# Kernel tuning notes

Measured on AMD Instinct MI355X. Metric: run time of the kernel, lower is better.

The kernel has to match this reference:

```python
import jax, jax.numpy as jnp
import numpy as np

B, S, N, D, H = 2, 64, 48, 128, 8
DH = D // H
_SCALE = 1.0 / float(np.sqrt(DH))


def _ln(x, g, b):
    m = jnp.mean(x, -1, keepdims=True)
    v = jnp.mean((x - m) ** 2, -1, keepdims=True)
    return (x - m) * jax.lax.rsqrt(v + 1e-5) * g + b


def setup_inputs() -> dict:
    key = jax.random.key(0)
    ks = jax.random.split(key, 40)
    rn = lambda i, shape, s=0.02: jax.random.normal(ks[i], shape, dtype=jnp.float32) * s
    inp = {
        'x': jax.random.normal(ks[0], (B, S, N, D), dtype=jnp.float32),
        'adjacency_matrix': jax.random.uniform(ks[1], (N, N), dtype=jnp.float32),
        'spatial_pos': rn(2, (1, N, D)),
        'temporal_pos': rn(3, (1, S, D)),
        'inter_w': rn(4, (H, DH, DH)),
        'conv_w1': rn(5, (D, D, 1)), 'conv_b1': jnp.zeros((D,), jnp.float32),
        'conv_w3': rn(6, (D, D, 3)), 'conv_b3': jnp.zeros((D,), jnp.float32),
        'conv_w5': rn(7, (D, D, 5)), 'conv_b5': jnp.zeros((D,), jnp.float32),
        'conv_w7': rn(8, (D, D, 7)), 'conv_b7': jnp.zeros((D,), jnp.float32),
        'sp_w0': rn(9, (D, D)), 'sp_b0': jnp.zeros((D,), jnp.float32),
        'sp_w1': rn(10, (D, D)), 'sp_b1': jnp.zeros((D,), jnp.float32),
        'sp_w2': rn(11, (D, D)), 'sp_b2': jnp.zeros((D,), jnp.float32),
        'attn_in_w': rn(12, (3 * D, D)), 'attn_in_b': jnp.zeros((3 * D,), jnp.float32),
        'attn_out_w': rn(13, (D, D)), 'attn_out_b': jnp.zeros((D,), jnp.float32),
        'gsp_w': rn(14, (D, 2 * D)), 'gsp_b': jnp.zeros((D,), jnp.float32),
        'gtm_w': rn(15, (D, 2 * D)), 'gtm_b': jnp.zeros((D,), jnp.float32),
        'gfu_w': rn(16, (D, 2 * D)), 'gfu_b': jnp.zeros((D,), jnp.float32),
        'ln1_g': jnp.ones((D,), jnp.float32), 'ln1_b': jnp.zeros((D,), jnp.float32),
        'ln2_g': jnp.ones((D,), jnp.float32), 'ln2_b': jnp.zeros((D,), jnp.float32),
        'ln3_g': jnp.ones((D,), jnp.float32), 'ln3_b': jnp.zeros((D,), jnp.float32),
    }
    return inp


def _forward(x, adjacency_matrix, spatial_pos, temporal_pos, inter_w,
             conv_w1, conv_b1, conv_w3, conv_b3, conv_w5, conv_b5, conv_w7, conv_b7,
             sp_w0, sp_b0, sp_w1, sp_b1, sp_w2, sp_b2,
             attn_in_w, attn_in_b, attn_out_w, attn_out_b,
             gsp_w, gsp_b, gtm_w, gtm_b, gfu_w, gfu_b,
             ln1_g, ln1_b, ln2_g, ln2_b, ln3_g, ln3_b):
    # positional encodings: spatial [1,N,D] broadcast over seq, temporal [1,S,D] over nodes
    x = x + spatial_pos[:, None] + temporal_pos[:, :, None]

    # ---- multi-scale temporal conv: [B*N, D, S] conv1d with k in {1,3,5,7} ----
    xt = x.transpose(0, 2, 3, 1).reshape(B * N, D, S)
    acc = None
    for w, b, k in ((conv_w1, conv_b1, 1), (conv_w3, conv_b3, 3), (conv_w5, conv_b5, 5), (conv_w7, conv_b7, 7)):
        o = jax.lax.conv_general_dilated(xt, w, (1,), [(k // 2, k // 2)],
                                         dimension_numbers=('NCH', 'OIH', 'NCH'))
        o = jax.nn.relu(o + b[None, :, None])
        acc = o if acc is None else acc + o
    tmp = (acc / 4.0).reshape(B, N, D, S).transpose(0, 3, 1, 2)  # [B,S,N,D]
    temporal = _ln(tmp + x, ln1_g, ln1_b)

    # ---- multi-hop spatial graph conv ----
    deg = adjacency_matrix.sum(1, keepdims=True)
    deg = jnp.where(deg == 0, 1.0, deg)
    nadj = adjacency_matrix / deg
    ap = nadj
    sacc = None
    for i, (w, b) in enumerate(((sp_w0, sp_b0), (sp_w1, sp_b1), (sp_w2, sp_b2))):
        c = jnp.einsum('mn,bsnd->bsmd', ap, x)
        c = jax.nn.relu(c @ w.T + b)
        sacc = c if sacc is None else sacc + c
        if i < 2:
            ap = ap @ nadj
    spatial = _ln(sacc / 3.0 + x, ln2_g, ln2_b)

    # ---- per-head bilinear interaction (batched over heads) ----
    th = temporal.reshape(B, S, N, H, DH)
    sh = spatial.reshape(B, S, N, H, DH)
    inter = jnp.einsum('bsnhi,hij,bsnhj->bsnhi', th, inter_w, sh).reshape(B, S, N, D)

    # ---- cross attention over flattened S*N tokens (torch MultiheadAttention math) ----
    L = S * N
    tf = temporal.reshape(B, L, D)
    sf = spatial.reshape(B, L, D)
    wq, wk, wv = attn_in_w[:D], attn_in_w[D:2 * D], attn_in_w[2 * D:]
    bq, bk, bv = attn_in_b[:D], attn_in_b[D:2 * D], attn_in_b[2 * D:]
    q = (tf @ wq.T + bq).reshape(B, L, H, DH)
    k_ = (sf @ wk.T + bk).reshape(B, L, H, DH)
    v = (sf @ wv.T + bv).reshape(B, L, H, DH)
    att = jax.nn.softmax(jnp.einsum('blhd,bmhd->bhlm', q, k_) * _SCALE, axis=-1)
    ao = jnp.einsum('bhlm,bmhd->blhd', att, v).reshape(B, L, D)
    cross = (ao @ attn_out_w.T + attn_out_b).reshape(B, S, N, D)

    # ---- adaptive gated fusion ----
    ig = jax.nn.sigmoid(jnp.concatenate([inter, x], -1) @ gsp_w.T + gsp_b)
    cg = jax.nn.sigmoid(jnp.concatenate([cross, x], -1) @ gtm_w.T + gtm_b)
    comb = ig * inter + cg * cross
    fg = jax.nn.sigmoid(jnp.concatenate([comb, x], -1) @ gfu_w.T + gfu_b)
    out = fg * comb + (1.0 - fg) * x
    return _ln(out, ln3_g, ln3_b)


def reference(x, adjacency_matrix, spatial_pos, temporal_pos, inter_w,
              conv_w1, conv_b1, conv_w3, conv_b3, conv_w5, conv_b5, conv_w7, conv_b7,
              sp_w0, sp_b0, sp_w1, sp_b1, sp_w2, sp_b2,
              attn_in_w, attn_in_b, attn_out_w, attn_out_b,
              gsp_w, gsp_b, gtm_w, gtm_b, gfu_w, gfu_b,
              ln1_g, ln1_b, ln2_g, ln2_b, ln3_g, ln3_b):
    return _forward(x, adjacency_matrix, spatial_pos, temporal_pos, inter_w,
                    conv_w1, conv_b1, conv_w3, conv_b3, conv_w5, conv_b5, conv_w7, conv_b7,
                    sp_w0, sp_b0, sp_w1, sp_b1, sp_w2, sp_b2,
                    attn_in_w, attn_in_b, attn_out_w, attn_out_b,
                    gsp_w, gsp_b, gtm_w, gtm_b, gfu_w, gfu_b,
                    ln1_g, ln1_b, ln2_g, ln2_b, ln3_g, ln3_b)
```

## Files before the change

kernel.cpp:

```cpp
#include <hip/hip_runtime.h>
#include <math.h>

typedef unsigned short ushort_t;
typedef unsigned int uint_t;
typedef float  float4_t  __attribute__((ext_vector_type(4)));
typedef short  short8_t  __attribute__((ext_vector_type(8)));
typedef short  short4_t  __attribute__((ext_vector_type(4)));

static constexpr int B_   = 2;
static constexpr int S_   = 64;
static constexpr int N_   = 48;
static constexpr int D_   = 128;
static constexpr int H_   = 8;
static constexpr int DH_  = 16;
static constexpr int L_   = S_ * N_;
static constexpr int TOK_ = B_ * L_;
static constexpr int F_   = TOK_ * D_;

__device__ __forceinline__ uint_t bf16rne(float f) {
  uint_t u = __float_as_uint(f);
  return (u + 0x7fffu + ((u >> 16) & 1u)) >> 16;
}
__device__ __forceinline__ uint_t cvtpk_bf16(float lo, float hi) {
  uint_t r;
  asm("v_cvt_pk_bf16_f32 %0, %1, %2" : "=v"(r) : "v"(lo), "v"(hi));
  return r;
}
__device__ __forceinline__ float sigmoidf_(float z) {
  return 1.0f / (1.0f + __expf(-z));
}

__global__ void k_posadd(const float* __restrict__ x, const float* __restrict__ sp,
                         const float* __restrict__ tp, float* __restrict__ xpe) {
  int idx = blockIdx.x * 256 + threadIdx.x;
  if (idx >= F_) return;
  int d  = idx & 127;
  int t2 = idx >> 7;
  int n  = t2 % 48;
  int t3 = t2 / 48;
  int s  = t3 & 63;
  xpe[idx] = x[idx] + sp[n * 128 + d] + tp[s * 128 + d];
}

__global__ void k_adjprep(const float* __restrict__ adj, ushort_t* __restrict__ apb) {
  __shared__ float degl[48];
  __shared__ float a1[2304];
  __shared__ float a2[2304];
  int tid = threadIdx.x;
  if (tid < 48) {
    float s = 0.f;
    for (int n = 0; n < 48; n++) s += adj[tid * 48 + n];
    degl[tid] = (s == 0.0f) ? 1.0f : s;
  }
  __syncthreads();
  for (int e = tid; e < 2304; e += 1024) {
    float v = adj[e] / degl[e / 48];
    a1[e] = v;
    apb[(e / 48) * 64 + (e % 48)] = (ushort_t)bf16rne(v);
  }
  __syncthreads();
  for (int e = tid; e < 2304; e += 1024) {
    int m = e / 48, n = e % 48;
    float s = 0.f;
    for (int k2 = 0; k2 < 48; k2++) s += a1[m * 48 + k2] * a1[k2 * 48 + n];
    a2[e] = s;
    apb[3072 + m * 64 + n] = (ushort_t)bf16rne(s);
  }
  __syncthreads();
  for (int e = tid; e < 2304; e += 1024) {
    int m = e / 48, n = e % 48;
    float s = 0.f;
    for (int k2 = 0; k2 < 48; k2++) s += a2[m * 48 + k2] * a1[k2 * 48 + n];
    apb[6144 + m * 64 + n] = (ushort_t)bf16rne(s);
  }
  for (int e = tid; e < 2304; e += 1024) {
    int hop = e / 768, rem = e % 768;
    apb[hop * 3072 + (rem / 16) * 64 + 48 + (rem % 16)] = 0;
  }
}

__global__ void k_wprep(const float* __restrict__ w1, const float* __restrict__ w3,
                        const float* __restrict__ w5, const float* __restrict__ w7,
                        ushort_t* __restrict__ wprep) {
  int idx = blockIdx.x * 256 + threadIdx.x;
  int p = idx >> 14;
  int rem = idx & 16383;
  int c = rem >> 7, i = rem & 127;
  float v;
  if (p == 0)       v = w1[c * 128 + i];
  else if (p < 4)   v = w3[(c * 128 + i) * 3 + (p - 1)];
  else if (p < 9)   v = w5[(c * 128 + i) * 5 + (p - 4)];
  else              v = w7[(c * 128 + i) * 7 + (p - 9)];
  wprep[idx] = (ushort_t)bf16rne(v);
}

__global__ void k_wprep2(const float* __restrict__ w0, const float* __restrict__ w1,
                         const float* __restrict__ w2, ushort_t* __restrict__ wsp) {
  int idx = blockIdx.x * 256 + threadIdx.x;
  if (idx >= 49152) return;
  int hop = idx >> 14, r = idx & 16383;
  const float* W = (hop == 0) ? w0 : ((hop == 1) ? w1 : w2);
  wsp[idx] = (ushort_t)bf16rne(W[r]);
}

__global__ void k_wprep3(const float* __restrict__ wo, const float* __restrict__ gsp,
                         const float* __restrict__ gtm, const float* __restrict__ gfu,
                         const float* __restrict__ wIn, ushort_t* __restrict__ wfin) {
  int idx = blockIdx.x * 256 + threadIdx.x;
  if (idx >= 163840) return;
  float v;
  if (idx < 16384)       v = wo[idx];
  else if (idx < 49152)  v = gsp[idx - 16384];
  else if (idx < 81920)  v = gtm[idx - 49152];
  else if (idx < 114688) v = gfu[idx - 81920];
  else                   v = wIn[idx - 114688];
  wfin[idx] = (ushort_t)bf16rne(v);
}

__global__ __launch_bounds__(256) void k_conv_mfma(
    const float* __restrict__ xpe, const ushort_t* __restrict__ wprep,
    const float* __restrict__ b1, const float* __restrict__ b3,
    const float* __restrict__ b5, const float* __restrict__ b7,
    float* __restrict__ out) {
  __shared__ ushort_t xl[38 * 128];
  char* xlb = (char*)xl;
  int blk = blockIdx.x;
  int bn = blk >> 2, chalf = (blk >> 1) & 1, thalf = blk & 1;
  int b = bn / 48, node = bn % 48;
  int t0 = thalf * 32;
  int tid = threadIdx.x;

  for (int seg = tid; seg < 608; seg += 256) {
    int row = seg >> 4, sidx = seg & 15;
    int gt = t0 + row - 3;
    int dst = row * 256 + ((sidx * 16) ^ ((row & 7) << 4));
    uint4 pk = make_uint4(0, 0, 0, 0);
    if (gt >= 0 && gt < 64) {
      const float* src = xpe + ((size_t)((b * 64 + gt) * 48 + node)) * 128 + sidx * 8;
      float4 f0 = ((const float4*)src)[0];
      float4 f1 = ((const float4*)src)[1];
      pk.x = bf16rne(f0.x) | (bf16rne(f0.y) << 16);
      pk.y = bf16rne(f0.z) | (bf16rne(f0.w) << 16);
      pk.z = bf16rne(f1.x) | (bf16rne(f1.y) << 16);
      pk.w = bf16rne(f1.z) | (bf16rne(f1.w) << 16);
    }
    *(uint4*)(xlb + dst) = pk;
  }
  __syncthreads();

  int w = tid >> 6, lane = tid & 63;
  int i16 = lane & 15, grp = lane >> 4;
  int grpoff = grp * 16;
  int c0 = chalf * 64 + w * 16;

  float4_t acc[4][2];
#pragma unroll
  for (int cv = 0; cv < 4; cv++)
#pragma unroll
    for (int tm = 0; tm < 2; tm++) acc[cv][tm] = (float4_t){0.f, 0.f, 0.f, 0.f};

  const int cid[16] = {0, 1, 1, 1, 2, 2, 2, 2, 2, 3, 3, 3, 3, 3, 3, 3};
  const int shf[16] = {0, -1, 0, 1, -2, -1, 0, 1, 2, -3, -2, -1, 0, 1, 2, 3};

#pragma unroll
  for (int p = 0; p < 16; p++) {
    int rb0 = 3 + shf[p] + i16;
#pragma unroll
    for (int ks = 0; ks < 4; ks++) {
      short8_t bfr = *(const short8_t*)(wprep + ((size_t)(p * 128 + c0 + i16)) * 128 + ks * 32 + grp * 8);
#pragma unroll
      for (int tm = 0; tm < 2; tm++) {
        int row = rb0 + tm * 16;
        int off = row * 256 + ((ks * 64 + grpoff) ^ ((row & 7) << 4));
        short8_t afr = *(const short8_t*)(xlb + off);
        acc[cid[p]][tm] = __builtin_amdgcn_mfma_f32_16x16x32_bf16(afr, bfr, acc[cid[p]][tm], 0, 0, 0);
      }
    }
  }

  int c = c0 + i16;
  float bias0 = b1[c], bias1 = b3[c], bias2 = b5[c], bias3 = b7[c];
#pragma unroll
  for (int tm = 0; tm < 2; tm++) {
#pragma unroll
    for (int r = 0; r < 4; r++) {
      int t = t0 + tm * 16 + grp * 4 + r;
      size_t gidx = ((size_t)((b * 64 + t) * 48 + node)) * 128 + c;
      float v = fmaxf(acc[0][tm][r] + bias0, 0.f) + fmaxf(acc[1][tm][r] + bias1, 0.f)
              + fmaxf(acc[2][tm][r] + bias2, 0.f) + fmaxf(acc[3][tm][r] + bias3, 0.f);
      out[gidx] = v * 0.25f + xpe[gidx];
    }
  }
}

__global__ void k_ln(const float* __restrict__ in, float* __restrict__ outp,
                     const float* __restrict__ g, const float* __restrict__ bb) {
  int row  = blockIdx.x * 4 + (threadIdx.x >> 6);
  int lane = threadIdx.x & 63;
  const float* r = in + row * 128;
  float v0 = r[lane], v1 = r[lane + 64];
  float s = v0 + v1;
#pragma unroll
  for (int m = 32; m; m >>= 1) s += __shfl_xor(s, m);
  float mean = s * (1.0f / 128.0f);
  float d0 = v0 - mean, d1 = v1 - mean;
  float q = d0 * d0 + d1 * d1;
#pragma unroll
  for (int m = 32; m; m >>= 1) q += __shfl_xor(q, m);
  float rstd = rsqrtf(q * (1.0f / 128.0f) + 1e-5f);
  outp[row * 128 + lane]      = d0 * rstd * g[lane]      + bb[lane];
  outp[row * 128 + lane + 64] = d1 * rstd * g[lane + 64] + bb[lane + 64];
}

__global__ __launch_bounds__(256) void k_spatial_mfma(
    const float* __restrict__ xpe, const ushort_t* __restrict__ apb,
    const ushort_t* __restrict__ wsp,
    const float* __restrict__ bb0, const float* __restrict__ bb1,
    const float* __restrict__ bb2, float* __restrict__ outp) {
  __shared__ ushort_t XT[128 * 64];
  __shared__ ushort_t Cl[48 * 128];
  char* XTb = (char*)XT;
  char* Clb = (char*)Cl;
  int bs = blockIdx.x;
  int tid = threadIdx.x;
  const float* xrow = xpe + (size_t)bs * 6144;

  for (int e = tid; e < 1024; e += 256)
    *(uint4*)(XTb + e * 16) = make_uint4(0, 0, 0, 0);
  __syncthreads();
  for (int e = tid; e < 1536; e += 256) {
    int node = e % 48, dq = e / 48;
    float4 xv = *(const float4*)(xrow + node * 128 + dq * 4);
    int d0 = dq * 4;
    *(ushort_t*)(XTb + (((d0 + 0) * 128 + node * 2) ^ (((d0 + 0) & 7) << 4))) = (ushort_t)bf16rne(xv.x);
    *(ushort_t*)(XTb + (((d0 + 1) * 128 + node * 2) ^ (((d0 + 1) & 7) << 4))) = (ushort_t)bf16rne(xv.y);
    *(ushort_t*)(XTb + (((d0 + 2) * 128 + node * 2) ^ (((d0 + 2) & 7) << 4))) = (ushort_t)bf16rne(xv.z);
    *(ushort_t*)(XTb + (((d0 + 3) * 128 + node * 2) ^ (((d0 + 3) & 7) << 4))) = (ushort_t)bf16rne(xv.w);
  }
  __syncthreads();

  int w = tid >> 6, lane = tid & 63;
  int i16 = lane & 15, g = lane >> 4;

  float4_t sacc[3][2];
#pragma unroll
  for (int mt = 0; mt < 3; mt++)
#pragma unroll
    for (int nt = 0; nt < 2; nt++) sacc[mt][nt] = (float4_t){0.f, 0.f, 0.f, 0.f};

  for (int hop = 0; hop < 3; hop++) {
    float4_t c1[2][3];
#pragma unroll
    for (int mt = 0; mt < 2; mt++)
#pragma unroll
      for (int nt = 0; nt < 3; nt++) c1[mt][nt] = (float4_t){0.f, 0.f, 0.f, 0.f};
#pragma unroll
    for (int kt = 0; kt < 2; kt++) {
#pragma unroll
      for (int mt = 0; mt < 2; mt++) {
        int arow = (w * 2 + mt) * 16 + i16;
        short8_t af = *(const short8_t*)(XTb + ((arow * 128 + (kt * 32 + 8 * g) * 2) ^ ((arow & 7) << 4)));
#pragma unroll
        for (int nt = 0; nt < 3; nt++) {
          short8_t bf = *(const short8_t*)(apb + hop * 3072 + (nt * 16 + i16) * 64 + kt * 32 + 8 * g);
          c1[mt][nt] = __builtin_amdgcn_mfma_f32_16x16x32_bf16(af, bf, c1[mt][nt], 0, 0, 0);
        }
      }
    }
    __syncthreads();
#pragma unroll
    for (int mt = 0; mt < 2; mt++) {
#pragma unroll
      for (int nt = 0; nt < 3; nt++) {
        int node = nt * 16 + i16;
        int d0 = (w * 2 + mt) * 16 + 4 * g;
        uint_t lo = cvtpk_bf16(c1[mt][nt][0], c1[mt][nt][1]);
        uint_t hi = cvtpk_bf16(c1[mt][nt][2], c1[mt][nt][3]);
        *(uint2*)(Clb + ((node * 256 + d0 * 2) ^ ((node & 7) << 4))) = make_uint2(lo, hi);
      }
    }
    __syncthreads();
    float4_t c2[3][2];
#pragma unroll
    for (int mt = 0; mt < 3; mt++)
#pragma unroll
      for (int nt = 0; nt < 2; nt++) c2[mt][nt] = (float4_t){0.f, 0.f, 0.f, 0.f};
#pragma unroll
    for (int kt = 0; kt < 4; kt++) {
#pragma unroll
      for (int mt = 0; mt < 3; mt++) {
        int arow = mt * 16 + i16;
        short8_t af = *(const short8_t*)(Clb + ((arow * 256 + (kt * 32 + 8 * g) * 2) ^ ((arow & 7) << 4)));
#pragma unroll
        for (int nt = 0; nt < 2; nt++) {
          int o = (w * 2 + nt) * 16 + i16;
          short8_t bf = *(const short8_t*)(wsp + ((size_t)(hop * 128 + o)) * 128 + kt * 32 + 8 * g);
          c2[mt][nt] = __builtin_amdgcn_mfma_f32_16x16x32_bf16(af, bf, c2[mt][nt], 0, 0, 0);
        }
      }
    }
    const float* Bs = (hop == 0) ? bb0 : ((hop == 1) ? bb1 : bb2);
#pragma unroll
    for (int nt = 0; nt < 2; nt++) {
      float bi = Bs[(w * 2 + nt) * 16 + i16];
#pragma unroll
      for (int mt = 0; mt < 3; mt++)
#pragma unroll
        for (int r = 0; r < 4; r++)
          sacc[mt][nt][r] += fmaxf(c2[mt][nt][r] + bi, 0.f);
    }
  }
  float* orow = outp + (size_t)bs * 6144;
#pragma unroll
  for (int mt = 0; mt < 3; mt++) {
#pragma unroll
    for (int nt = 0; nt < 2; nt++) {
#pragma unroll
      for (int r = 0; r < 4; r++) {
        int node = mt * 16 + 4 * g + r;
        int o = (w * 2 + nt) * 16 + i16;
        orow[node * 128 + o] = sacc[mt][nt][r] * (1.0f / 3.0f) + xrow[node * 128 + o];
      }
    }
  }
}

__global__ void k_inter(const float* __restrict__ temporal, const float* __restrict__ spatial,
                        const float* __restrict__ iw, float* __restrict__ outp) {
  __shared__ float sl[128];
  int tok = blockIdx.x;
  int tid = threadIdx.x;
  sl[tid] = spatial[tok * 128 + tid];
  float tv = temporal[tok * 128 + tid];
  __syncthreads();
  int h = tid >> 4;
  const float* W = iw + tid * 16;
  float s = 0.f;
#pragma unroll
  for (int j = 0; j < 16; j++) s += W[j] * sl[h * 16 + j];
  outp[tok * 128 + tid] = tv * s;
}

__global__ __launch_bounds__(256) void k_qkv_mfma(
    const float* __restrict__ temporal, const float* __restrict__ spatial,
    const ushort_t* __restrict__ wqkv, const float* __restrict__ bIn,
    ushort_t* __restrict__ qb, ushort_t* __restrict__ kb, ushort_t* __restrict__ vtb) {
  __shared__ ushort_t bufT[32 * 128];
  __shared__ ushort_t bufS[32 * 128];
  char* T_ = (char*)bufT;
  char* S_ = (char*)bufS;
  int tok0 = blockIdx.x * 32;
  int tid = threadIdx.x;

  for (int seg = tid; seg < 512; seg += 256) {
    int row = seg >> 4, c8 = (seg & 15) * 8;
    int dst = (row * 256 + c8 * 2) ^ ((row & 7) << 4);
    size_t gbase = (size_t)(tok0 + row) * 128 + c8;
    {
      float4 f0 = *(const float4*)(temporal + gbase);
      float4 f1 = *(const float4*)(temporal + gbase + 4);
      *(uint4*)(T_ + dst) = make_uint4(cvtpk_bf16(f0.x, f0.y), cvtpk_bf16(f0.z, f0.w),
                                       cvtpk_bf16(f1.x, f1.y), cvtpk_bf16(f1.z, f1.w));
    }
    {
      float4 f0 = *(const float4*)(spatial + gbase);
      float4 f1 = *(const float4*)(spatial + gbase + 4);
      *(uint4*)(S_ + dst) = make_uint4(cvtpk_bf16(f0.x, f0.y), cvtpk_bf16(f0.z, f0.w),
                                       cvtpk_bf16(f1.x, f1.y), cvtpk_bf16(f1.z, f1.w));
    }
  }
  __syncthreads();

  int w = tid >> 6, lane = tid & 63;
  int i16 = lane & 15, g = lane >> 4;
  int mt = w >> 1, nh = w & 1;
  int mrow = mt * 16 + i16;
  int b = tok0 / 3072, l0 = tok0 % 3072;
  const float QSCALE = 0.25f * 1.4426950408889634f;

  float4_t accQ[4], accK[4], accV[4];
#pragma unroll
  for (int nt = 0; nt < 4; nt++) {
    accQ[nt] = (float4_t){0.f, 0.f, 0.f, 0.f};
    accK[nt] = (float4_t){0.f, 0.f, 0.f, 0.f};
    accV[nt] = (float4_t){0.f, 0.f, 0.f, 0.f};
  }

#pragma unroll
  for (int kt = 0; kt < 4; kt++) {
    short8_t af = *(const short8_t*)(T_ + ((mrow * 256 + (kt * 32 + 8 * g) * 2) ^ ((mrow & 7) << 4)));
#pragma unroll
    for (int nt = 0; nt < 4; nt++) {
      int o = nh * 64 + nt * 16 + i16;
      short8_t bf = *(const short8_t*)(wqkv + (size_t)o * 128 + kt * 32 + 8 * g);
      accQ[nt] = __builtin_amdgcn_mfma_f32_16x16x32_bf16(af, bf, accQ[nt], 0, 0, 0);
    }
  }
#pragma unroll
  for (int kt = 0; kt < 4; kt++) {
    short8_t af = *(const short8_t*)(S_ + ((mrow * 256 + (kt * 32 + 8 * g) * 2) ^ ((mrow & 7) << 4)));
#pragma unroll
    for (int nt = 0; nt < 4; nt++) {
      int o = nh * 64 + nt * 16 + i16;
      short8_t bfk = *(const short8_t*)(wqkv + (size_t)(128 + o) * 128 + kt * 32 + 8 * g);
      short8_t bfv = *(const short8_t*)(wqkv + (size_t)(256 + o) * 128 + kt * 32 + 8 * g);
      accK[nt] = __builtin_amdgcn_mfma_f32_16x16x32_bf16(af, bfk, accK[nt], 0, 0, 0);
      accV[nt] = __builtin_amdgcn_mfma_f32_16x16x32_bf16(af, bfv, accV[nt], 0, 0, 0);
    }
  }

#pragma unroll
  for (int nt = 0; nt < 4; nt++) {
    int o = nh * 64 + nt * 16 + i16;
    int h = o >> 4, dh = o & 15;
    int bh = b * 8 + h;
    float bq = bIn[o], bk = bIn[128 + o], bv = bIn[256 + o];
#pragma unroll
    for (int r = 0; r < 4; r++) {
      int l = l0 + mt * 16 + 4 * g + r;
      qb[((size_t)bh * 3072 + l) * 16 + dh] = (ushort_t)bf16rne((accQ[nt][r] + bq) * QSCALE);
      kb[((size_t)bh * 3072 + l) * 16 + dh] = (ushort_t)bf16rne(accK[nt][r] + bk);
      vtb[((size_t)bh * 16 + dh) * 3072 + l] = (ushort_t)bf16rne(accV[nt][r] + bv);
    }
  }
}

#define ATTN_CORE(K0, K1, V0, V1)                                                    \
  {                                                                                  \
    float4_t S0 = __builtin_amdgcn_mfma_f32_16x16x32_bf16(K0, qf, (float4_t){0.f,0.f,0.f,0.f}, 0, 0, 0); \
    float4_t S1 = __builtin_amdgcn_mfma_f32_16x16x32_bf16(K1, qf, (float4_t){0.f,0.f,0.f,0.f}, 0, 0, 0); \
    float p0 = exp2f(S0[0]), p1 = exp2f(S0[1]), p2 = exp2f(S0[2]), p3 = exp2f(S0[3]); \
    float p4 = exp2f(S1[0]), p5 = exp2f(S1[1]), p6 = exp2f(S1[2]), p7 = exp2f(S1[3]); \
    lsum += ((p0 + p1) + (p2 + p3)) + ((p4 + p5) + (p6 + p7));                       \
    union { uint_t u[4]; short8_t s; } pp;                                           \
    pp.u[0] = cvtpk_bf16(p0, p1); pp.u[1] = cvtpk_bf16(p2, p3);                      \
    pp.u[2] = cvtpk_bf16(p4, p5); pp.u[3] = cvtpk_bf16(p6, p7);                      \
    union { short4_t s4[2]; short8_t s8; } vv; vv.s4[0] = V0; vv.s4[1] = V1;         \
    Ot = __builtin_amdgcn_mfma_f32_16x16x32_bf16(vv.s8, pp.s, Ot, 0, 0, 0);          \
  }

__global__ __launch_bounds__(256) void k_attn_mfma(
    const ushort_t* __restrict__ qb, const ushort_t* __restrict__ kb,
    const ushort_t* __restrict__ vtb, float* __restrict__ aob) {
  int blk = blockIdx.x;
  int bh = blk / 48, qt = blk % 48;
  int w = threadIdx.x >> 6, lane = threadIdx.x & 63;
  int i16 = lane & 15, g = lane >> 4;
  int q = qt * 64 + w * 16 + i16;

  const ushort_t* qbase = qb + (size_t)bh * 3072 * 16;
  const ushort_t* kfp = kb + (size_t)bh * 3072 * 16 + i16 * 16 + (g & 1) * 8;
  const ushort_t* vrow = vtb + ((size_t)bh * 16 + i16) * 3072 + 4 * g;

  short8_t qf = {0, 0, 0, 0, 0, 0, 0, 0};
  if (g < 2) qf = *(const short8_t*)(qbase + q * 16 + g * 8);

  float4_t Ot = {0.f, 0.f, 0.f, 0.f};
  float lsum = 0.f;

  short8_t kA0 = *(const short8_t*)(kfp + 0);
  short8_t kA1 = *(const short8_t*)(kfp + 256);
  short4_t vA0 = *(const short4_t*)(vrow + 0);
  short4_t vA1 = *(const short4_t*)(vrow + 16);
  short8_t kB0 = *(const short8_t*)(kfp + 512);
  short8_t kB1 = *(const short8_t*)(kfp + 768);
  short4_t vB0 = *(const short4_t*)(vrow + 32);
  short4_t vB1 = *(const short4_t*)(vrow + 48);

  for (int kt = 0; kt < 3072; kt += 64) {
    {
      short8_t k0 = kA0, k1 = kA1; short4_t v0 = vA0, v1 = vA1;
      int pt = kt + 64;
      kA0 = *(const short8_t*)(kfp + pt * 16);
      kA1 = *(const short8_t*)(kfp + pt * 16 + 256);
      vA0 = *(const short4_t*)(vrow + pt);
      vA1 = *(const short4_t*)(vrow + pt + 16);
      ATTN_CORE(k0, k1, v0, v1);
    }
    {
      short8_t k0 = kB0, k1 = kB1; short4_t v0 = vB0, v1 = vB1;
      int pt = kt + 96;
      kB0 = *(const short8_t*)(kfp + pt * 16);
      kB1 = *(const short8_t*)(kfp + pt * 16 + 256);
      vB0 = *(const short4_t*)(vrow + pt);
      vB1 = *(const short4_t*)(vrow + pt + 16);
      ATTN_CORE(k0, k1, v0, v1);
    }
  }

  lsum += __shfl_xor(lsum, 16);
  lsum += __shfl_xor(lsum, 32);
  float inv = 1.0f / lsum;
  int b = bh >> 3, h = bh & 7;
  float* orow = aob + ((size_t)b * 3072 + q) * 128 + h * 16;
#pragma unroll
  for (int r = 0; r < 4; r++) orow[4 * g + r] = Ot[r] * inv;
}

__global__ __launch_bounds__(256) void k_final_mfma(
    const float* __restrict__ aob, const float* __restrict__ xpe,
    const float* __restrict__ inter, const ushort_t* __restrict__ wfin,
    const float* __restrict__ bo,
    const float* __restrict__ gspb, const float* __restrict__ gtmb,
    const float* __restrict__ gfub,
    const float* __restrict__ g3, const float* __restrict__ b3,
    float* __restrict__ outp) {
  __shared__ ushort_t bufA[32 * 128];
  __shared__ ushort_t bufX[32 * 128];
  __shared__ ushort_t bufI[32 * 128];
  __shared__ float mpart[32][2], spart[32][2];
  char* A_ = (char*)bufA;
  char* X_ = (char*)bufX;
  char* I_ = (char*)bufI;
  int tok0 = blockIdx.x * 32;
  int tid = threadIdx.x;

  for (int seg = tid; seg < 512; seg += 256) {
    int row = seg >> 4, c8 = (seg & 15) * 8;
    int dst = (row * 256 + c8 * 2) ^ ((row & 7) << 4);
    size_t gbase = (size_t)(tok0 + row) * 128 + c8;
    {
      float4 f0 = *(const float4*)(aob + gbase);
      float4 f1 = *(const float4*)(aob + gbase + 4);
      uint4 pk = make_uint4(cvtpk_bf16(f0.x, f0.y), cvtpk_bf16(f0.z, f0.w),
                            cvtpk_bf16(f1.x, f1.y), cvtpk_bf16(f1.z, f1.w));
      *(uint4*)(A_ + dst) = pk;
    }
    {
      float4 f0 = *(const float4*)(xpe + gbase);
      float4 f1 = *(const float4*)(xpe + gbase + 4);
      uint4 pk = make_uint4(cvtpk_bf16(f0.x, f0.y), cvtpk_bf16(f0.z, f0.w),
                            cvtpk_bf16(f1.x, f1.y), cvtpk_bf16(f1.z, f1.w));
      *(uint4*)(X_ + dst) = pk;
    }
    {
      float4 f0 = *(const float4*)(inter + gbase);
      float4 f1 = *(const float4*)(inter + gbase + 4);
      uint4 pk = make_uint4(cvtpk_bf16(f0.x, f0.y), cvtpk_bf16(f0.z, f0.w),
                            cvtpk_bf16(f1.x, f1.y), cvtpk_bf16(f1.z, f1.w));
      *(uint4*)(I_ + dst) = pk;
    }
  }
  __syncthreads();

  int w = tid >> 6, lane = tid & 63;
  int i16 = lane & 15, g = lane >> 4;
  int mt = w >> 1, nh = w & 1;
  int mrow = mt * 16 + i16;

#define GATE_GEMM(ACT, WBASE, ACC)                                                            \
  {                                                                                           \
    _Pragma("unroll")                                                                         \
    for (int kt = 0; kt < 4; kt++) {                                                          \
      short8_t af = *(const short8_t*)((ACT) + ((mrow * 256 + (kt * 32 + 8 * g) * 2) ^ ((mrow & 7) << 4))); \
      _Pragma("unroll")                                                                       \
      for (int nt = 0; nt < 4; nt++) {                                                        \
        int o = nh * 64 + nt * 16 + i16;                                                      \
        short8_t bf = *(const short8_t*)(wfin + (WBASE) + (size_t)o * 256 + kt * 32 + 8 * g); \
        ACC[nt] = __builtin_amdgcn_mfma_f32_16x16x32_bf16(af, bf, ACC[nt], 0, 0, 0);          \
      }                                                                                       \
    }                                                                                         \
    _Pragma("unroll")                                                                         \
    for (int kt = 0; kt < 4; kt++) {                                                          \
      short8_t af = *(const short8_t*)(X_ + ((mrow * 256 + (kt * 32 + 8 * g) * 2) ^ ((mrow & 7) << 4))); \
      _Pragma("unroll")                                                                       \
      for (int nt = 0; nt < 4; nt++) {                                                        \
        int o = nh * 64 + nt * 16 + i16;                                                      \
        short8_t bf = *(const short8_t*)(wfin + (WBASE) + (size_t)o * 256 + 128 + kt * 32 + 8 * g); \
        ACC[nt] = __builtin_amdgcn_mfma_f32_16x16x32_bf16(af, bf, ACC[nt], 0, 0, 0);          \
      }                                                                                       \
    }                                                                                         \
  }

  float4_t accC[4];
#pragma unroll
  for (int nt = 0; nt < 4; nt++) accC[nt] = (float4_t){0.f, 0.f, 0.f, 0.f};
#pragma unroll
  for (int kt = 0; kt < 4; kt++) {
    short8_t af = *(const short8_t*)(A_ + ((mrow * 256 + (kt * 32 + 8 * g) * 2) ^ ((mrow & 7) << 4)));
#pragma unroll
    for (int nt = 0; nt < 4; nt++) {
      int o = nh * 64 + nt * 16 + i16;
      short8_t bf = *(const short8_t*)(wfin + (size_t)o * 128 + kt * 32 + 8 * g);
      accC[nt] = __builtin_amdgcn_mfma_f32_16x16x32_bf16(af, bf, accC[nt], 0, 0, 0);
    }
  }

  float4_t accIg[4];
#pragma unroll
  for (int nt = 0; nt < 4; nt++) accIg[nt] = (float4_t){0.f, 0.f, 0.f, 0.f};
  GATE_GEMM(I_, 16384, accIg);

  float crossv[4][4];
#pragma unroll
  for (int nt = 0; nt < 4; nt++) {
    float bv = bo[nh * 64 + nt * 16 + i16];
#pragma unroll
    for (int r = 0; r < 4; r++) crossv[nt][r] = accC[nt][r] + bv;
  }
  __syncthreads();
#pragma unroll
  for (int nt = 0; nt < 4; nt++) {
#pragma unroll
    for (int r = 0; r < 4; r++) {
      int trow = mt * 16 + 4 * g + r;
      int col = nh * 64 + nt * 16 + i16;
      *(ushort_t*)(A_ + ((trow * 256 + col * 2) ^ ((trow & 7) << 4))) = (ushort_t)bf16rne(crossv[nt][r]);
    }
  }
  __syncthreads();

  float4_t accCg[4];
#pragma unroll
  for (int nt = 0; nt < 4; nt++) accCg[nt] = (float4_t){0.f, 0.f, 0.f, 0.f};
  GATE_GEMM(A_, 49152, accCg);

  float comb[4][4];
#pragma unroll
  for (int nt = 0; nt < 4; nt++) {
    int o = nh * 64 + nt * 16 + i16;
    float bg1 = gspb[o], bg2 = gtmb[o];
#pragma unroll
    for (int r = 0; r < 4; r++) {
      int trow = mt * 16 + 4 * g + r;
      float iv = inter[(size_t)(tok0 + trow) * 128 + o];
      float igv = sigmoidf_(accIg[nt][r] + bg1);
      float cgv = sigmoidf_(accCg[nt][r] + bg2);
      comb[nt][r] = igv * iv + cgv * crossv[nt][r];
    }
  }
  __syncthreads();
#pragma unroll
  for (int nt = 0; nt < 4; nt++) {
#pragma unroll
    for (int r = 0; r < 4; r++) {
      int trow = mt * 16 + 4 * g + r;
      int col = nh * 64 + nt * 16 + i16;
      *(ushort_t*)(A_ + ((trow * 256 + col * 2) ^ ((trow & 7) << 4))) = (ushort_t)bf16rne(comb[nt][r]);
    }
  }
  __syncthreads();

  float4_t accFg[4];
#pragma unroll
  for (int nt = 0; nt < 4; nt++) accFg[nt] = (float4_t){0.f, 0.f, 0.f, 0.f};
  GATE_GEMM(A_, 81920, accFg);

  float outv[4][4];
  float psum[4] = {0.f, 0.f, 0.f, 0.f}, psq[4] = {0.f, 0.f, 0.f, 0.f};
#pragma unroll
  for (int nt = 0; nt < 4; nt++) {
    int o = nh * 64 + nt * 16 + i16;
    float bgf = gfub[o];
#pragma unroll
    for (int r = 0; r < 4; r++) {
      int trow = mt * 16 + 4 * g + r;
      float xv = xpe[(size_t)(tok0 + trow) * 128 + o];
      float fgv = sigmoidf_(accFg[nt][r] + bgf);
      float ov = fgv * comb[nt][r] + (1.0f - fgv) * xv;
      outv[nt][r] = ov;
      psum[r] += ov;
      psq[r] += ov * ov;
    }
  }
#pragma unroll
  for (int r = 0; r < 4; r++) {
#pragma unroll
    for (int mk = 1; mk < 16; mk <<= 1) {
      psum[r] += __shfl_xor(psum[r], mk);
      psq[r]  += __shfl_xor(psq[r], mk);
    }
  }
  if (i16 == 0) {
#pragma unroll
    for (int r = 0; r < 4; r++) {
      int tl = mt * 16 + 4 * g + r;
      mpart[tl][nh] = psum[r];
      spart[tl][nh] = psq[r];
    }
  }
  __syncthreads();
  float gv[4], bv3[4];
#pragma unroll
  for (int nt = 0; nt < 4; nt++) {
    int o = nh * 64 + nt * 16 + i16;
    gv[nt] = g3[o];
    bv3[nt] = b3[o];
  }
#pragma unroll
  for (int r = 0; r < 4; r++) {
    int tl = mt * 16 + 4 * g + r;
    float mean = (mpart[tl][0] + mpart[tl][1]) * (1.0f / 128.0f);
    float var = (spart[tl][0] + spart[tl][1]) * (1.0f / 128.0f) - mean * mean;
    float rstd = rsqrtf(var + 1e-5f);
#pragma unroll
    for (int nt = 0; nt < 4; nt++) {
      int o = nh * 64 + nt * 16 + i16;
      outp[(size_t)(tok0 + tl) * 128 + o] = (outv[nt][r] - mean) * rstd * gv[nt] + bv3[nt];
    }
  }
#undef GATE_GEMM
}

extern "C" void kernel_launch(void* const* d_in, const int* in_sizes, int n_in,
                              void* d_out, int out_size, void* d_ws, size_t ws_size,
                              hipStream_t stream) {
  (void)in_sizes; (void)n_in; (void)out_size; (void)ws_size;
  const float* x    = (const float*)d_in[0];
  const float* adj  = (const float*)d_in[1];
  const float* spos = (const float*)d_in[2];
  const float* tpos = (const float*)d_in[3];
  const float* iw   = (const float*)d_in[4];
  const float* w1   = (const float*)d_in[5];
  const float* b1   = (const float*)d_in[6];
  const float* w3   = (const float*)d_in[7];
  const float* b3   = (const float*)d_in[8];
  const float* w5   = (const float*)d_in[9];
  const float* b5   = (const float*)d_in[10];
  const float* w7   = (const float*)d_in[11];
  const float* b7   = (const float*)d_in[12];
  const float* spw0 = (const float*)d_in[13];
  const float* spb0 = (const float*)d_in[14];
  const float* spw1 = (const float*)d_in[15];
  const float* spb1 = (const float*)d_in[16];
  const float* spw2 = (const float*)d_in[17];
  const float* spb2 = (const float*)d_in[18];
  const float* wIn  = (const float*)d_in[19];
  const float* bIn  = (const float*)d_in[20];
  const float* wOut = (const float*)d_in[21];
  const float* bOut = (const float*)d_in[22];
  const float* gspw = (const float*)d_in[23];
  const float* gspb = (const float*)d_in[24];
  const float* gtmw = (const float*)d_in[25];
  const float* gtmb = (const float*)d_in[26];
  const float* gfuw = (const float*)d_in[27];
  const float* gfub = (const float*)d_in[28];
  const float* ln1g = (const float*)d_in[29];
  const float* ln1b = (const float*)d_in[30];
  const float* ln2g = (const float*)d_in[31];
  const float* ln2b = (const float*)d_in[32];
  const float* ln3g = (const float*)d_in[33];
  const float* ln3b = (const float*)d_in[34];

  float* ws = (float*)d_ws;
  float* xpe      = ws + 0 * (size_t)F_;
  float* tconv    = ws + 1 * (size_t)F_;
  float* temporal = ws + 2 * (size_t)F_;
  float* sppre    = ws + 3 * (size_t)F_;
  float* spatial  = ws + 4 * (size_t)F_;
  float* inter    = ws + 5 * (size_t)F_;
  ushort_t* qb    = (ushort_t*)(ws + 6 * (size_t)F_);
  ushort_t* kbb   = qb + (size_t)16 * 3072 * 16;
  ushort_t* vtb   = (ushort_t*)(ws + 7 * (size_t)F_);
  ushort_t* wprep = vtb + (size_t)786432;
  ushort_t* wsp   = wprep + (size_t)262144;
  ushort_t* wfin  = wsp + (size_t)49152;
  ushort_t* wqkv  = wfin + (size_t)114688;
  ushort_t* apb   = wfin + (size_t)163840;
  float* aob = tconv;

  k_posadd<<<F_ / 256, 256, 0, stream>>>(x, spos, tpos, xpe);
  k_adjprep<<<1, 1024, 0, stream>>>(adj, apb);
  k_wprep<<<1024, 256, 0, stream>>>(w1, w3, w5, w7, wprep);
  k_wprep2<<<192, 256, 0, stream>>>(spw0, spw1, spw2, wsp);
  k_wprep3<<<640, 256, 0, stream>>>(wOut, gspw, gtmw, gfuw, wIn, wfin);
  k_conv_mfma<<<384, 256, 0, stream>>>(xpe, wprep, b1, b3, b5, b7, tconv);
  k_ln<<<TOK_ / 4, 256, 0, stream>>>(tconv, temporal, ln1g, ln1b);
  k_spatial_mfma<<<B_ * S_, 256, 0, stream>>>(xpe, apb, wsp, spb0, spb1, spb2, sppre);
  k_ln<<<TOK_ / 4, 256, 0, stream>>>(sppre, spatial, ln2g, ln2b);
  k_inter<<<TOK_, 128, 0, stream>>>(temporal, spatial, iw, inter);
  k_qkv_mfma<<<TOK_ / 32, 256, 0, stream>>>(temporal, spatial, wqkv, bIn, qb, kbb, vtb);
  k_attn_mfma<<<768, 256, 0, stream>>>(qb, kbb, vtb, aob);
  k_final_mfma<<<TOK_ / 32, 256, 0, stream>>>(aob, xpe, inter, wfin, bOut,
                                              gspb, gtmb, gfub, ln3g, ln3b,
                                              (float*)d_out);
}
```

Baseline: 181.6 us.

## Merge prep and layernorm launches, fold inter product into QKV kernel

The position-add and three weight-conversion kernels become one multi-role launch. The two layernorm launches become a single grid that covers both inputs. The per-token inter-head bilinear product moves into the QKV kernel, reusing the bf16 tiles already staged in shared memory. This removes several launches and one full read of the temporal and spatial tensors. In exchange, the inter product is now computed from bf16-rounded inputs instead of fp32, which lowers precision.

```diff
diff --git a/kernel.cpp b/kernel.cpp
--- a/kernel.cpp
+++ b/kernel.cpp
@@ -30,16 +30,52 @@
   return 1.0f / (1.0f + __expf(-z));
 }
 
-__global__ void k_posadd(const float* __restrict__ x, const float* __restrict__ sp,
-                         const float* __restrict__ tp, float* __restrict__ xpe) {
-  int idx = blockIdx.x * 256 + threadIdx.x;
-  if (idx >= F_) return;
-  int d  = idx & 127;
-  int t2 = idx >> 7;
-  int n  = t2 % 48;
-  int t3 = t2 / 48;
-  int s  = t3 & 63;
-  xpe[idx] = x[idx] + sp[n * 128 + d] + tp[s * 128 + d];
+__global__ void k_prep(const float* __restrict__ x, const float* __restrict__ sp,
+                       const float* __restrict__ tp, float* __restrict__ xpe,
+                       const float* __restrict__ w1, const float* __restrict__ w3,
+                       const float* __restrict__ w5, const float* __restrict__ w7,
+                       ushort_t* __restrict__ wprep,
+                       const float* __restrict__ sw0, const float* __restrict__ sw1,
+                       const float* __restrict__ sw2, ushort_t* __restrict__ wsp,
+                       const float* __restrict__ wo, const float* __restrict__ gsp,
+                       const float* __restrict__ gtm, const float* __restrict__ gfu,
+                       const float* __restrict__ wIn, ushort_t* __restrict__ wfin) {
+  int blk = blockIdx.x;
+  int tid = threadIdx.x;
+  if (blk < 3072) {
+    int idx = blk * 256 + tid;
+    int d  = idx & 127;
+    int t2 = idx >> 7;
+    int n  = t2 % 48;
+    int t3 = t2 / 48;
+    int s  = t3 & 63;
+    xpe[idx] = x[idx] + sp[n * 128 + d] + tp[s * 128 + d];
+  } else if (blk < 4096) {
+    int idx = (blk - 3072) * 256 + tid;
+    int p = idx >> 14;
+    int rem = idx & 16383;
+    int c = rem >> 7, i = rem & 127;
+    float v;
+    if (p == 0)       v = w1[c * 128 + i];
+    else if (p < 4)   v = w3[(c * 128 + i) * 3 + (p - 1)];
+    else if (p < 9)   v = w5[(c * 128 + i) * 5 + (p - 4)];
+    else              v = w7[(c * 128 + i) * 7 + (p - 9)];
+    wprep[idx] = (ushort_t)bf16rne(v);
+  } else if (blk < 4288) {
+    int idx = (blk - 4096) * 256 + tid;
+    int hop = idx >> 14, r = idx & 16383;
+    const float* W = (hop == 0) ? sw0 : ((hop == 1) ? sw1 : sw2);
+    wsp[idx] = (ushort_t)bf16rne(W[r]);
+  } else {
+    int idx = (blk - 4288) * 256 + tid;
+    float v;
+    if (idx < 16384)       v = wo[idx];
+    else if (idx < 49152)  v = gsp[idx - 16384];
+    else if (idx < 81920)  v = gtm[idx - 49152];
+    else if (idx < 114688) v = gfu[idx - 81920];
+    else                   v = wIn[idx - 114688];
+    wfin[idx] = (ushort_t)bf16rne(v);
+  }
 }
 
 __global__ void k_adjprep(const float* __restrict__ adj, ushort_t* __restrict__ apb) {
@@ -77,44 +113,6 @@
     int hop = e / 768, rem = e % 768;
     apb[hop * 3072 + (rem / 16) * 64 + 48 + (rem % 16)] = 0;
   }
-}
-
-__global__ void k_wprep(const float* __restrict__ w1, const float* __restrict__ w3,
-                        const float* __restrict__ w5, const float* __restrict__ w7,
-                        ushort_t* __restrict__ wprep) {
-  int idx = blockIdx.x * 256 + threadIdx.x;
-  int p = idx >> 14;
-  int rem = idx & 16383;
-  int c = rem >> 7, i = rem & 127;
-  float v;
-  if (p == 0)       v = w1[c * 128 + i];
-  else if (p < 4)   v = w3[(c * 128 + i) * 3 + (p - 1)];
-  else if (p < 9)   v = w5[(c * 128 + i) * 5 + (p - 4)];
-  else              v = w7[(c * 128 + i) * 7 + (p - 9)];
-  wprep[idx] = (ushort_t)bf16rne(v);
-}
-
-__global__ void k_wprep2(const float* __restrict__ w0, const float* __restrict__ w1,
-                         const float* __restrict__ w2, ushort_t* __restrict__ wsp) {
-  int idx = blockIdx.x * 256 + threadIdx.x;
-  if (idx >= 49152) return;
-  int hop = idx >> 14, r = idx & 16383;
-  const float* W = (hop == 0) ? w0 : ((hop == 1) ? w1 : w2);
-  wsp[idx] = (ushort_t)bf16rne(W[r]);
-}
-
-__global__ void k_wprep3(const float* __restrict__ wo, const float* __restrict__ gsp,
-                         const float* __restrict__ gtm, const float* __restrict__ gfu,
-                         const float* __restrict__ wIn, ushort_t* __restrict__ wfin) {
-  int idx = blockIdx.x * 256 + threadIdx.x;
-  if (idx >= 163840) return;
-  float v;
-  if (idx < 16384)       v = wo[idx];
-  else if (idx < 49152)  v = gsp[idx - 16384];
-  else if (idx < 81920)  v = gtm[idx - 49152];
-  else if (idx < 114688) v = gfu[idx - 81920];
-  else                   v = wIn[idx - 114688];
-  wfin[idx] = (ushort_t)bf16rne(v);
 }
 
 __global__ __launch_bounds__(256) void k_conv_mfma(
@@ -193,9 +191,17 @@
   }
 }
 
-__global__ void k_ln(const float* __restrict__ in, float* __restrict__ outp,
-                     const float* __restrict__ g, const float* __restrict__ bb) {
-  int row  = blockIdx.x * 4 + (threadIdx.x >> 6);
+__global__ void k_lnx2(const float* __restrict__ in1, float* __restrict__ out1,
+                       const float* __restrict__ g1, const float* __restrict__ b1,
+                       const float* __restrict__ in2, float* __restrict__ out2,
+                       const float* __restrict__ g2, const float* __restrict__ b2) {
+  int blk = blockIdx.x;
+  const float* in  = (blk < 1536) ? in1  : in2;
+  float* outp      = (blk < 1536) ? out1 : out2;
+  const float* g   = (blk < 1536) ? g1   : g2;
+  const float* bb  = (blk < 1536) ? b1   : b2;
+  int rblk = (blk < 1536) ? blk : (blk - 1536);
+  int row  = rblk * 4 + (threadIdx.x >> 6);
   int lane = threadIdx.x & 63;
   const float* r = in + row * 128;
   float v0 = r[lane], v1 = r[lane + 64];
@@ -325,26 +331,12 @@
   }
 }
 
-__global__ void k_inter(const float* __restrict__ temporal, const float* __restrict__ spatial,
-                        const float* __restrict__ iw, float* __restrict__ outp) {
-  __shared__ float sl[128];
-  int tok = blockIdx.x;
-  int tid = threadIdx.x;
-  sl[tid] = spatial[tok * 128 + tid];
-  float tv = temporal[tok * 128 + tid];
-  __syncthreads();
-  int h = tid >> 4;
-  const float* W = iw + tid * 16;
-  float s = 0.f;
-#pragma unroll
-  for (int j = 0; j < 16; j++) s += W[j] * sl[h * 16 + j];
-  outp[tok * 128 + tid] = tv * s;
-}
-
 __global__ __launch_bounds__(256) void k_qkv_mfma(
     const float* __restrict__ temporal, const float* __restrict__ spatial,
     const ushort_t* __restrict__ wqkv, const float* __restrict__ bIn,
-    ushort_t* __restrict__ qb, ushort_t* __restrict__ kb, ushort_t* __restrict__ vtb) {
+    const float* __restrict__ iw,
+    ushort_t* __restrict__ qb, ushort_t* __restrict__ kb, ushort_t* __restrict__ vtb,
+    float* __restrict__ interp) {
   __shared__ ushort_t bufT[32 * 128];
   __shared__ ushort_t bufS[32 * 128];
   char* T_ = (char*)bufT;
@@ -421,6 +413,36 @@
       qb[((size_t)bh * 3072 + l) * 16 + dh] = (ushort_t)bf16rne((accQ[nt][r] + bq) * QSCALE);
       kb[((size_t)bh * 3072 + l) * 16 + dh] = (ushort_t)bf16rne(accK[nt][r] + bk);
       vtb[((size_t)bh * 16 + dh) * 3072 + l] = (ushort_t)bf16rne(accV[nt][r] + bv);
+    }
+  }
+
+  {
+    int o = tid & 127, th = tid >> 7;
+    int jb = o & ~15;
+    float W[16];
+    const float4* W4 = (const float4*)(iw + o * 16);
+#pragma unroll
+    for (int j4 = 0; j4 < 4; j4++) {
+      float4 wv = W4[j4];
+      W[j4 * 4 + 0] = wv.x; W[j4 * 4 + 1] = wv.y;
+      W[j4 * 4 + 2] = wv.z; W[j4 * 4 + 3] = wv.w;
+    }
+    for (int tk = 0; tk < 16; tk++) {
+      int row = th * 16 + tk;
+      int sw = (row & 7) << 4;
+      uint4 h0 = *(const uint4*)(S_ + ((row * 256 + jb * 2) ^ sw));
+      uint4 h1 = *(const uint4*)(S_ + ((row * 256 + jb * 2 + 16) ^ sw));
+      uint_t su[8] = {h0.x, h0.y, h0.z, h0.w, h1.x, h1.y, h1.z, h1.w};
+      float s = 0.f;
+#pragma unroll
+      for (int j = 0; j < 8; j++) {
+        float lo = __uint_as_float(su[j] << 16);
+        float hi = __uint_as_float(su[j] & 0xFFFF0000u);
+        s += W[2 * j] * lo + W[2 * j + 1] * hi;
+      }
+      uint_t tu = *(const ushort_t*)(T_ + ((row * 256 + o * 2) ^ sw));
+      float tv = __uint_as_float((uint_t)tu << 16);
+      interp[(size_t)(tok0 + row) * 128 + o] = tv * s;
     }
   }
 }
@@ -759,17 +781,17 @@
   ushort_t* apb   = wfin + (size_t)163840;
   float* aob = tconv;
 
-  k_posadd<<<F_ / 256, 256, 0, stream>>>(x, spos, tpos, xpe);
+  k_prep<<<4928, 256, 0, stream>>>(x, spos, tpos, xpe,
+                                   w1, w3, w5, w7, wprep,
+                                   spw0, spw1, spw2, wsp,
+                                   wOut, gspw, gtmw, gfuw, wIn, wfin);
   k_adjprep<<<1, 1024, 0, stream>>>(adj, apb);
-  k_wprep<<<1024, 256, 0, stream>>>(w1, w3, w5, w7, wprep);
-  k_wprep2<<<192, 256, 0, stream>>>(spw0, spw1, spw2, wsp);
-  k_wprep3<<<640, 256, 0, stream>>>(wOut, gspw, gtmw, gfuw, wIn, wfin);
   k_conv_mfma<<<384, 256, 0, stream>>>(xpe, wprep, b1, b3, b5, b7, tconv);
-  k_ln<<<TOK_ / 4, 256, 0, stream>>>(tconv, temporal, ln1g, ln1b);
   k_spatial_mfma<<<B_ * S_, 256, 0, stream>>>(xpe, apb, wsp, spb0, spb1, spb2, sppre);
-  k_ln<<<TOK_ / 4, 256, 0, stream>>>(sppre, spatial, ln2g, ln2b);
-  k_inter<<<TOK_, 128, 0, stream>>>(temporal, spatial, iw, inter);
-  k_qkv_mfma<<<TOK_ / 32, 256, 0, stream>>>(temporal, spatial, wqkv, bIn, qb, kbb, vtb);
+  k_lnx2<<<3072, 256, 0, stream>>>(tconv, temporal, ln1g, ln1b,
+                                   sppre, spatial, ln2g, ln2b);
+  k_qkv_mfma<<<TOK_ / 32, 256, 0, stream>>>(temporal, spatial, wqkv, bIn, iw,
+                                            qb, kbb, vtb, inter);
   k_attn_mfma<<<768, 256, 0, stream>>>(qb, kbb, vtb, aob);
   k_final_mfma<<<TOK_ / 32, 256, 0, stream>>>(aob, xpe, inter, wfin, bOut,
                                               gspb, gtmb, gfub, ln3g, ln3b,
```

Measured after the change: 170.7 us (median of 2 runs). 1.06x faster.
